# Performance work log

Measured on AMD Instinct MI355X. Metric: run time of the kernel, lower is better.

Reference implementation:

```python
import jax, jax.numpy as jnp
import numpy as np

S, N, E = 12, 16384, 262144        # timesteps, nodes, edges per timestep
DIN = DOUT = H = 128               # gcn in/out dim == lstm hidden (required by module)
B = 64                             # batch_size; N % B == 0


def setup_inputs() -> dict:
    key = jax.random.key(0)
    ks = jax.random.split(key, 10)
    return {
        "adj_indices": jax.random.randint(ks[0], (S, 2, E), 0, N, dtype=jnp.int32),
        "adj_values": jax.random.uniform(ks[1], (S, E), dtype=jnp.float32),
        "xs": jax.random.normal(ks[2], (S, N, DIN), dtype=jnp.float32),
        "gcn_weight": jax.random.normal(ks[3], (DIN, DOUT), dtype=jnp.float32) * 0.05,
        "gcn_bias": jnp.zeros((DOUT,), jnp.float32),
        "w_ih": jax.random.normal(ks[4], (4 * H, DOUT), dtype=jnp.float32) * 0.05,
        "w_hh": jax.random.normal(ks[5], (4 * H, H), dtype=jnp.float32) * 0.05,
        "b_ih": jnp.zeros((4 * H,), jnp.float32),
        "b_hh": jnp.zeros((4 * H,), jnp.float32),
        "h0": jax.random.normal(ks[6], (B, H), dtype=jnp.float32),
        "c0": jax.random.normal(ks[7], (B, H), dtype=jnp.float32),
    }


def reference(adj_indices, adj_values, xs, gcn_weight, gcn_bias,
              w_ih, w_hh, b_ih, b_hh, h0, c0):
    # --- GCN per timestep: relu(sparse_A @ (X @ W) + b) ---
    def gcn(idx, vals, x):
        support = x @ gcn_weight                      # [N, DOUT]
        msg = vals[:, None] * support[idx[1]]         # gather cols -> [E, DOUT]
        out = jax.ops.segment_sum(msg, idx[0], num_segments=N)  # scatter rows
        return jax.nn.relu(out + gcn_bias)

    cur = jax.vmap(gcn)(adj_indices, adj_values, xs)  # [S, N, DOUT]
    seq = cur.reshape(-1, B, DOUT)                    # [T=S*N/B, B, H]

    # --- single-layer LSTM (torch gate order: i, f, g, o) ---
    def step(carry, x_t):
        h, c = carry
        gates = x_t @ w_ih.T + b_ih + h @ w_hh.T + b_hh   # [B, 4H]
        i, f, g, o = jnp.split(gates, 4, axis=-1)
        c = jax.nn.sigmoid(f) * c + jax.nn.sigmoid(i) * jnp.tanh(g)
        h = jax.nn.sigmoid(o) * jnp.tanh(c)
        return (h, c), h

    _, hs = jax.lax.scan(step, (h0, c0), seq)         # [T, B, H]
    return hs
```

## Files before the change

kernel.cpp:

```cpp
#include <hip/hip_runtime.h>
#include <cstdint>
#include <cstddef>

#define SS 12
#define NN 16384
#define EE 262144
#define TT 3072

typedef _Float16 h2_t __attribute__((ext_vector_type(2)));
typedef short bf16x8 __attribute__((ext_vector_type(8)));
typedef float floatx4 __attribute__((ext_vector_type(4)));
typedef unsigned short ushortx8 __attribute__((ext_vector_type(8)));

__device__ __forceinline__ float fast_sig(float x) {
    float e = __builtin_amdgcn_exp2f(-1.442695041f * x);
    return __builtin_amdgcn_rcpf(1.f + e);
}
__device__ __forceinline__ float fast_tanh(float x) {
    float e = __builtin_amdgcn_exp2f(2.885390082f * x);
    return 1.f - 2.f * __builtin_amdgcn_rcpf(e + 1.f);
}
__device__ __forceinline__ unsigned short f2bf(float f) {
    unsigned int x = __float_as_uint(f);
    unsigned int r = (x + 0x7FFFu + ((x >> 16) & 1u)) >> 16;
    return (unsigned short)r;
}
__device__ __forceinline__ float bf2f(unsigned short u) {
    return __uint_as_float(((unsigned int)u) << 16);
}
__device__ __forceinline__ h2_t u2h(unsigned int u) {
    union { unsigned int u; h2_t h; } c; c.u = u; return c.h;
}

__global__ void k_zero(int* __restrict__ p) {
    p[blockIdx.x * 256 + threadIdx.x] = 0;
}

__global__ void k_count(const int* __restrict__ adj, int* __restrict__ counts) {
    int i = blockIdx.x * 256 + threadIdx.x;
    int t = i / EE, e = i - t * EE;
    int dst = adj[(size_t)t * 2 * EE + e];
    atomicAdd(&counts[t * NN + dst], 1);
}

__global__ void k_scan(const int* __restrict__ counts, int* __restrict__ offs,
                       int* __restrict__ cursor) {
    __shared__ int sums[1024];
    int t = blockIdx.x, tid = threadIdx.x;
    const int per = NN / 1024;
    int base = t * NN + tid * per;
    int local[16];
    int s = 0;
#pragma unroll
    for (int i = 0; i < per; i++) { local[i] = counts[base + i]; s += local[i]; }
    sums[tid] = s;
    __syncthreads();
    for (int off = 1; off < 1024; off <<= 1) {
        int v = (tid >= off) ? sums[tid - off] : 0;
        __syncthreads();
        sums[tid] += v;
        __syncthreads();
    }
    int run = sums[tid] - s;
#pragma unroll
    for (int i = 0; i < per; i++) { offs[base + i] = run; cursor[base + i] = run; run += local[i]; }
}

__global__ void k_scatter(const int* __restrict__ adj, const float* __restrict__ vals,
                          int* __restrict__ cursor, int2* __restrict__ edges) {
    int i = blockIdx.x * 256 + threadIdx.x;
    int t = i / EE, e = i - t * EE;
    int dst = adj[(size_t)t * 2 * EE + e];
    int src = adj[(size_t)t * 2 * EE + EE + e];
    float v = vals[(size_t)t * EE + e];
    int p = atomicAdd(&cursor[t * NN + dst], 1);
    edges[(size_t)t * EE + p] = make_int2(src, __float_as_int(v));
}

__global__ __launch_bounds__(256) void k_support(const float* __restrict__ xs,
                                                 const float* __restrict__ W,
                                                 unsigned short* __restrict__ sup) {
    __shared__ float Ash[64][128];
    __shared__ float Wsh[128][128];
    int tid = threadIdx.x;
    size_t rowbase = (size_t)blockIdx.x * 64;
    const float4* xa = (const float4*)(xs + rowbase * 128);
    float4* As = (float4*)&Ash[0][0];
#pragma unroll
    for (int q = 0; q < 8; q++) As[tid + q * 256] = xa[tid + q * 256];
    const float4* wg = (const float4*)W;
    float4* Ws = (float4*)&Wsh[0][0];
#pragma unroll
    for (int q = 0; q < 16; q++) Ws[tid + q * 256] = wg[tid + q * 256];
    __syncthreads();
    int jg = tid & 31, rg = tid >> 5;
    float acc[8][4];
#pragma unroll
    for (int i = 0; i < 8; i++)
#pragma unroll
        for (int j = 0; j < 4; j++) acc[i][j] = 0.f;
    for (int k4 = 0; k4 < 128; k4 += 4) {
        float4 a[8];
#pragma unroll
        for (int i = 0; i < 8; i++) a[i] = *(const float4*)&Ash[rg * 8 + i][k4];
#pragma unroll
        for (int kk = 0; kk < 4; kk++) {
            float4 wv = *(const float4*)&Wsh[k4 + kk][jg * 4];
#pragma unroll
            for (int i = 0; i < 8; i++) {
                float av = (kk == 0) ? a[i].x : (kk == 1) ? a[i].y : (kk == 2) ? a[i].z : a[i].w;
                acc[i][0] += av * wv.x; acc[i][1] += av * wv.y;
                acc[i][2] += av * wv.z; acc[i][3] += av * wv.w;
            }
        }
    }
#pragma unroll
    for (int i = 0; i < 8; i++) {
        ushort4 o;
        o.x = f2bf(acc[i][0]); o.y = f2bf(acc[i][1]);
        o.z = f2bf(acc[i][2]); o.w = f2bf(acc[i][3]);
        *(ushort4*)&sup[(rowbase + rg * 8 + i) * 128 + jg * 4] = o;
    }
}

__global__ __launch_bounds__(256) void k_gather(const int2* __restrict__ edges,
                         const int* __restrict__ offs,
                         const int* __restrict__ ends,
                         const unsigned short* __restrict__ sup,
                         const float* __restrict__ bias,
                         unsigned short* __restrict__ cur) {
    int bn = blockIdx.x * 4 + (threadIdx.x >> 6);
    bn = __builtin_amdgcn_readfirstlane(bn);
    int t = bn >> 14;
    int l = threadIdx.x & 63;
    int beg = offs[bn];
    int end = ends[bn];
    const unsigned short* supt = sup + (size_t)t * NN * 128;
    const int2* eg = edges + (size_t)t * EE;
    float acc0 = 0.f, acc1 = 0.f;
    int p = beg;
    for (; p + 3 < end; p += 4) {
        int2 e0 = eg[p], e1 = eg[p + 1], e2 = eg[p + 2], e3 = eg[p + 3];
        unsigned int u0 = *(const unsigned int*)&supt[(size_t)e0.x * 128 + 2 * l];
        unsigned int u1 = *(const unsigned int*)&supt[(size_t)e1.x * 128 + 2 * l];
        unsigned int u2 = *(const unsigned int*)&supt[(size_t)e2.x * 128 + 2 * l];
        unsigned int u3 = *(const unsigned int*)&supt[(size_t)e3.x * 128 + 2 * l];
        float w0 = __int_as_float(e0.y), w1 = __int_as_float(e1.y);
        float w2 = __int_as_float(e2.y), w3 = __int_as_float(e3.y);
        acc0 += w0 * bf2f((unsigned short)u0); acc1 += w0 * bf2f((unsigned short)(u0 >> 16));
        acc0 += w1 * bf2f((unsigned short)u1); acc1 += w1 * bf2f((unsigned short)(u1 >> 16));
        acc0 += w2 * bf2f((unsigned short)u2); acc1 += w2 * bf2f((unsigned short)(u2 >> 16));
        acc0 += w3 * bf2f((unsigned short)u3); acc1 += w3 * bf2f((unsigned short)(u3 >> 16));
    }
    for (; p < end; p++) {
        int2 e0 = eg[p];
        unsigned int u0 = *(const unsigned int*)&supt[(size_t)e0.x * 128 + 2 * l];
        float w0 = __int_as_float(e0.y);
        acc0 += w0 * bf2f((unsigned short)u0);
        acc1 += w0 * bf2f((unsigned short)(u0 >> 16));
    }
    float r0 = acc0 + bias[2 * l];
    float r1 = acc1 + bias[2 * l + 1];
    ushort2 o;
    o.x = f2bf(r0 > 0.f ? r0 : 0.f);
    o.y = f2bf(r1 > 0.f ? r1 : 0.f);
    *(ushort2*)&cur[(size_t)bn * 128 + 2 * l] = o;
}

__global__ __launch_bounds__(256) void k_xgates(const unsigned short* __restrict__ cur,
                                                const float* __restrict__ wih,
                                                const float* __restrict__ bih,
                                                const float* __restrict__ bhh,
                                                unsigned short* __restrict__ gx) {
    __shared__ __align__(16) unsigned short At[64][136];
    __shared__ __align__(16) unsigned short Bt[64][136];
    int tid = threadIdx.x;
    size_t rowbase = (size_t)blockIdx.x * 64;
    int gbase = blockIdx.y * 64;
#pragma unroll
    for (int q = 0; q < 4; q++) {
        int idx = tid + q * 256;
        int r = idx >> 4;
        int cc = (idx & 15) * 8;
        *(ushortx8*)&At[r][cc] = *(const ushortx8*)&cur[(rowbase + r) * 128 + cc];
    }
#pragma unroll
    for (int q = 0; q < 8; q++) {
        int idx = tid + q * 256;
        int r = idx >> 5;
        int c4 = (idx & 31) * 4;
        float4 v = *(const float4*)&wih[(size_t)(gbase + r) * 128 + c4];
        ushort4 o;
        o.x = f2bf(v.x); o.y = f2bf(v.y); o.z = f2bf(v.z); o.w = f2bf(v.w);
        *(ushort4*)&Bt[r][c4] = o;
    }
    __syncthreads();
    int wave = tid >> 6, lane = tid & 63;
    int m0 = wave * 16;
    int rin = lane & 15;
    int koff = (lane >> 4) * 8;
    floatx4 acc[4];
#pragma unroll
    for (int n = 0; n < 4; n++) acc[n] = (floatx4){0.f, 0.f, 0.f, 0.f};
#pragma unroll
    for (int kc = 0; kc < 4; kc++) {
        bf16x8 a = *(const bf16x8*)&At[m0 + rin][kc * 32 + koff];
#pragma unroll
        for (int n = 0; n < 4; n++) {
            bf16x8 b = *(const bf16x8*)&Bt[n * 16 + rin][kc * 32 + koff];
            acc[n] = __builtin_amdgcn_mfma_f32_16x16x32_bf16(a, b, acc[n], 0, 0, 0);
        }
    }
    int rq = (lane >> 4) * 4;
#pragma unroll
    for (int n = 0; n < 4; n++) {
        int gcol = gbase + n * 16 + rin;
        float bs = bih[gcol] + bhh[gcol];
#pragma unroll
        for (int i = 0; i < 4; i++) {
            size_t row = rowbase + m0 + rq + i;
            gx[row * 512 + gcol] = f2bf(acc[n][i] + bs);
        }
    }
}

__global__ __launch_bounds__(256, 1) void k_lstm(const unsigned short* __restrict__ gx,
                                                 const float* __restrict__ whh,
                                                 const float* __restrict__ h0,
                                                 const float* __restrict__ c0,
                                                 float* __restrict__ out) {
    __shared__ __align__(8) _Float16 hsh[128];
    __shared__ float gsh[512];
    int b = blockIdx.x, tid = threadIdx.x;
    int g1 = tid + 256;

    h2_t w0[64], w1[64];
    {
        const float4* r0 = (const float4*)(whh + (size_t)tid * 128);
        const float4* r1 = (const float4*)(whh + (size_t)g1 * 128);
#pragma unroll
        for (int q = 0; q < 32; q++) {
            float4 v = r0[q];
            h2_t p0; p0.x = (_Float16)v.x; p0.y = (_Float16)v.y;
            h2_t p1; p1.x = (_Float16)v.z; p1.y = (_Float16)v.w;
            w0[2 * q] = p0; w0[2 * q + 1] = p1;
        }
#pragma unroll
        for (int q = 0; q < 32; q++) {
            float4 v = r1[q];
            h2_t p0; p0.x = (_Float16)v.x; p0.y = (_Float16)v.y;
            h2_t p1; p1.x = (_Float16)v.z; p1.y = (_Float16)v.w;
            w1[2 * q] = p0; w1[2 * q + 1] = p1;
        }
    }
    float c = 0.f;
    if (tid < 128) {
        hsh[tid] = (_Float16)h0[(size_t)b * 128 + tid];
        c = c0[(size_t)b * 128 + tid];
    }
    __syncthreads();

    unsigned short nA0 = gx[(size_t)b * 512 + tid];
    unsigned short nA1 = gx[(size_t)b * 512 + g1];
    unsigned short nB0 = gx[((size_t)64 + b) * 512 + tid];
    unsigned short nB1 = gx[((size_t)64 + b) * 512 + g1];

    int lane = tid & 63;
    float hh[8];
    for (int t8 = 0; t8 < TT; t8 += 8) {
#pragma unroll
        for (int q = 0; q < 8; q++) {
            int t = t8 + q;
            float px0 = bf2f(nA0), px1 = bf2f(nA1);
            int tp2 = (t + 2 < TT) ? t + 2 : TT - 1;
            const unsigned short* gp = gx + ((size_t)tp2 * 64 + b) * 512;
            unsigned short nC0 = gp[tid];
            unsigned short nC1 = gp[g1];
            unsigned int hv = *(const unsigned int*)&hsh[lane * 2];
            float a00 = 0.f, a01 = 0.f, a10 = 0.f, a11 = 0.f;
#pragma unroll
            for (int mm = 0; mm < 64; mm += 2) {
                unsigned int s0 = __builtin_amdgcn_readlane(hv, mm);
                unsigned int s1 = __builtin_amdgcn_readlane(hv, mm + 1);
                a00 = __builtin_amdgcn_fdot2(w0[mm], u2h(s0), a00, false);
                a10 = __builtin_amdgcn_fdot2(w1[mm], u2h(s0), a10, false);
                a01 = __builtin_amdgcn_fdot2(w0[mm + 1], u2h(s1), a01, false);
                a11 = __builtin_amdgcn_fdot2(w1[mm + 1], u2h(s1), a11, false);
            }
            float r0 = a00 + a01 + px0;
            float r1 = a10 + a11 + px1;
            float act0 = fast_sig(r0);
            float act1 = (tid < 128) ? fast_tanh(r1) : fast_sig(r1);
            gsh[tid] = act0;
            gsh[g1] = act1;
            __syncthreads();
            if (tid < 128) {
                float ai = gsh[tid];
                float af = gsh[tid + 128];
                float ag = gsh[tid + 256];
                float ao = gsh[tid + 384];
                c = af * c + ai * ag;
                float hn = ao * fast_tanh(c);
                hh[q] = hn;
                hsh[tid] = (_Float16)hn;
            }
            __syncthreads();
            nA0 = nB0; nA1 = nB1; nB0 = nC0; nB1 = nC1;
        }
        if (tid < 128) {
#pragma unroll
            for (int q = 0; q < 8; q++)
                out[((size_t)(t8 + q) * 64 + b) * 128 + tid] = hh[q];
        }
    }
}

extern "C" void kernel_launch(void* const* d_in, const int* in_sizes, int n_in,
                              void* d_out, int out_size, void* d_ws, size_t ws_size,
                              hipStream_t stream) {
    const int* adj    = (const int*)d_in[0];
    const float* vals = (const float*)d_in[1];
    const float* xs   = (const float*)d_in[2];
    const float* gw   = (const float*)d_in[3];
    const float* gb   = (const float*)d_in[4];
    const float* wih  = (const float*)d_in[5];
    const float* whh  = (const float*)d_in[6];
    const float* bih  = (const float*)d_in[7];
    const float* bhh  = (const float*)d_in[8];
    const float* h0   = (const float*)d_in[9];
    const float* c0   = (const float*)d_in[10];
    float* out = (float*)d_out;

    char* ws = (char*)d_ws;
    unsigned short* cur = (unsigned short*)(ws);
    unsigned short* gx  = (unsigned short*)(ws + 50331648);
    unsigned short* sup = (unsigned short*)(ws + 50331648);
    int* counts         = (int*)(ws + 100663296);
    int* offs           = (int*)(ws + 101449728);
    int* cursor         = (int*)(ws + 102236160);
    int2* edges         = (int2*)(ws + 103022592);

    k_zero<<<(SS * NN) / 256, 256, 0, stream>>>(counts);
    k_count<<<(SS * EE) / 256, 256, 0, stream>>>(adj, counts);
    k_scan<<<SS, 1024, 0, stream>>>(counts, offs, cursor);
    k_scatter<<<(SS * EE) / 256, 256, 0, stream>>>(adj, vals, cursor, edges);
    k_support<<<(SS * NN) / 64, 256, 0, stream>>>(xs, gw, sup);
    k_gather<<<(SS * NN) / 4, 256, 0, stream>>>(edges, offs, cursor, sup, gb, cur);
    k_xgates<<<dim3((SS * NN) / 64, 8), 256, 0, stream>>>(cur, wih, bih, bhh, gx);
    k_lstm<<<64, 256, 0, stream>>>(gx, whh, h0, c0, out);
}
```

Before: 2.804 ms.

## Pair LSTM gates across adjacent lanes with DPP to drop a barrier per step

Gate rows are redistributed so each even/odd lane pair holds all four gates (i,f,g,o) of one hidden unit. The pair exchanges activations with a DPP quad-permute instead of going through shared memory, and the gx buffer is rewritten in a matching permuted column layout. Double-buffering the h vector in shared memory lets each timestep use one __syncthreads instead of two. Output is written directly each step rather than batched, and every lane now carries a cell state, with tanh computed as a scaled sigmoid.

Measured after the change: 2.564 ms. -8.6%, faster.

```diff
diff --git a/kernel.cpp b/kernel.cpp
--- a/kernel.cpp
+++ b/kernel.cpp
@@ -30,6 +30,10 @@
 }
 __device__ __forceinline__ h2_t u2h(unsigned int u) {
     union { unsigned int u; h2_t h; } c; c.u = u; return c.h;
+}
+__device__ __forceinline__ float dpp_xor1(float x) {
+    int i = __builtin_amdgcn_mov_dpp(__float_as_int(x), 0xB1, 0xF, 0xF, true);
+    return __int_as_float(i);
 }
 
 __global__ void k_zero(int* __restrict__ p) {
@@ -216,10 +220,12 @@
     for (int n = 0; n < 4; n++) {
         int gcol = gbase + n * 16 + rin;
         float bs = bih[gcol] + bhh[gcol];
+        int qg = gcol >> 7, jj = gcol & 127;
+        int slot = ((qg >> 1) << 8) | ((jj >> 5) << 6) | ((jj & 31) << 1) | (qg & 1);
 #pragma unroll
         for (int i = 0; i < 4; i++) {
             size_t row = rowbase + m0 + rq + i;
-            gx[row * 512 + gcol] = f2bf(acc[n][i] + bs);
+            gx[row * 512 + slot] = f2bf(acc[n][i] + bs);
         }
     }
 }
@@ -229,90 +235,88 @@
                                                  const float* __restrict__ h0,
                                                  const float* __restrict__ c0,
                                                  float* __restrict__ out) {
-    __shared__ __align__(8) _Float16 hsh[128];
-    __shared__ float gsh[512];
+    __shared__ __align__(8) _Float16 hsh[2][128];
     int b = blockIdx.x, tid = threadIdx.x;
-    int g1 = tid + 256;
+    int l = tid & 63, w = tid >> 6;
+    int j = w * 32 + (l >> 1);
+    bool even = (l & 1) == 0;
+    int gate0 = even ? j : 128 + j;
+    int gate1 = even ? 256 + j : 384 + j;
+    float Ss = even ? 2.f : 1.f;
+    float Aa = even ? 2.f : 1.f;
+    float Bb = even ? -1.f : 0.f;
 
     h2_t w0[64], w1[64];
     {
-        const float4* r0 = (const float4*)(whh + (size_t)tid * 128);
-        const float4* r1 = (const float4*)(whh + (size_t)g1 * 128);
+        const float4* r0p = (const float4*)(whh + (size_t)gate0 * 128);
+        const float4* r1p = (const float4*)(whh + (size_t)gate1 * 128);
 #pragma unroll
         for (int q = 0; q < 32; q++) {
-            float4 v = r0[q];
+            float4 v = r0p[q];
             h2_t p0; p0.x = (_Float16)v.x; p0.y = (_Float16)v.y;
             h2_t p1; p1.x = (_Float16)v.z; p1.y = (_Float16)v.w;
             w0[2 * q] = p0; w0[2 * q + 1] = p1;
         }
 #pragma unroll
         for (int q = 0; q < 32; q++) {
-            float4 v = r1[q];
+            float4 v = r1p[q];
             h2_t p0; p0.x = (_Float16)v.x; p0.y = (_Float16)v.y;
             h2_t p1; p1.x = (_Float16)v.z; p1.y = (_Float16)v.w;
             w1[2 * q] = p0; w1[2 * q + 1] = p1;
         }
     }
-    float c = 0.f;
-    if (tid < 128) {
-        hsh[tid] = (_Float16)h0[(size_t)b * 128 + tid];
-        c = c0[(size_t)b * 128 + tid];
-    }
+    float c = c0[(size_t)b * 128 + j];
+    if (tid < 128) hsh[0][tid] = (_Float16)h0[(size_t)b * 128 + tid];
     __syncthreads();
 
     unsigned short nA0 = gx[(size_t)b * 512 + tid];
-    unsigned short nA1 = gx[(size_t)b * 512 + g1];
+    unsigned short nA1 = gx[(size_t)b * 512 + 256 + tid];
     unsigned short nB0 = gx[((size_t)64 + b) * 512 + tid];
-    unsigned short nB1 = gx[((size_t)64 + b) * 512 + g1];
-
-    int lane = tid & 63;
-    float hh[8];
-    for (int t8 = 0; t8 < TT; t8 += 8) {
-#pragma unroll
-        for (int q = 0; q < 8; q++) {
-            int t = t8 + q;
-            float px0 = bf2f(nA0), px1 = bf2f(nA1);
-            int tp2 = (t + 2 < TT) ? t + 2 : TT - 1;
-            const unsigned short* gp = gx + ((size_t)tp2 * 64 + b) * 512;
-            unsigned short nC0 = gp[tid];
-            unsigned short nC1 = gp[g1];
-            unsigned int hv = *(const unsigned int*)&hsh[lane * 2];
-            float a00 = 0.f, a01 = 0.f, a10 = 0.f, a11 = 0.f;
-#pragma unroll
-            for (int mm = 0; mm < 64; mm += 2) {
-                unsigned int s0 = __builtin_amdgcn_readlane(hv, mm);
-                unsigned int s1 = __builtin_amdgcn_readlane(hv, mm + 1);
-                a00 = __builtin_amdgcn_fdot2(w0[mm], u2h(s0), a00, false);
-                a10 = __builtin_amdgcn_fdot2(w1[mm], u2h(s0), a10, false);
-                a01 = __builtin_amdgcn_fdot2(w0[mm + 1], u2h(s1), a01, false);
-                a11 = __builtin_amdgcn_fdot2(w1[mm + 1], u2h(s1), a11, false);
-            }
-            float r0 = a00 + a01 + px0;
-            float r1 = a10 + a11 + px1;
-            float act0 = fast_sig(r0);
-            float act1 = (tid < 128) ? fast_tanh(r1) : fast_sig(r1);
-            gsh[tid] = act0;
-            gsh[g1] = act1;
-            __syncthreads();
-            if (tid < 128) {
-                float ai = gsh[tid];
-                float af = gsh[tid + 128];
-                float ag = gsh[tid + 256];
-                float ao = gsh[tid + 384];
-                c = af * c + ai * ag;
-                float hn = ao * fast_tanh(c);
-                hh[q] = hn;
-                hsh[tid] = (_Float16)hn;
-            }
-            __syncthreads();
-            nA0 = nB0; nA1 = nB1; nB0 = nC0; nB1 = nC1;
-        }
-        if (tid < 128) {
-#pragma unroll
-            for (int q = 0; q < 8; q++)
-                out[((size_t)(t8 + q) * 64 + b) * 128 + tid] = hh[q];
-        }
-    }
+    unsigned short nB1 = gx[((size_t)64 + b) * 512 + 256 + tid];
+
+#define LSTM_STEP(T, RD, WR)                                               \
+    {                                                                      \
+        unsigned int hv = *(const unsigned int*)&hsh[RD][2 * l];           \
+        float px0 = bf2f(nA0), px1 = bf2f(nA1);                            \
+        int tp2 = ((T) + 2 < TT) ? (T) + 2 : TT - 1;                       \
+        const unsigned short* gp = gx + ((size_t)tp2 * 64 + b) * 512;      \
+        unsigned short nC0 = gp[tid];                                      \
+        unsigned short nC1 = gp[tid + 256];                                \
+        float a00 = 0.f, a01 = 0.f, a10 = 0.f, a11 = 0.f;                  \
+        _Pragma("unroll")                                                  \
+        for (int mm = 0; mm < 64; mm += 2) {                               \
+            unsigned int s0 = __builtin_amdgcn_readlane(hv, mm);           \
+            unsigned int s1 = __builtin_amdgcn_readlane(hv, mm + 1);       \
+            a00 = __builtin_amdgcn_fdot2(w0[mm], u2h(s0), a00, false);     \
+            a10 = __builtin_amdgcn_fdot2(w1[mm], u2h(s0), a10, false);     \
+            a01 = __builtin_amdgcn_fdot2(w0[mm + 1], u2h(s1), a01, false); \
+            a11 = __builtin_amdgcn_fdot2(w1[mm + 1], u2h(s1), a11, false); \
+        }                                                                  \
+        float r0 = a00 + a01 + px0;                                        \
+        float r1 = a10 + a11 + px1;                                        \
+        float act0 = fast_sig(r0);                                         \
+        float act1 = Aa * fast_sig(Ss * r1) + Bb;                          \
+        float q0 = dpp_xor1(act0);                                         \
+        float q1 = dpp_xor1(act1);                                         \
+        float gi = even ? act0 : q0;                                       \
+        float gf = even ? q0 : act0;                                       \
+        float gg = even ? act1 : q1;                                       \
+        float go = even ? q1 : act1;                                       \
+        c = gf * c + gi * gg;                                              \
+        float hn = go * fast_tanh(c);                                      \
+        if (even) {                                                        \
+            hsh[WR][j] = (_Float16)hn;                                     \
+            out[((size_t)(T) * 64 + b) * 128 + j] = hn;                    \
+        }                                                                  \
+        __syncthreads();                                                   \
+        nA0 = nB0; nA1 = nB1; nB0 = nC0; nB1 = nC1;                        \
+    }
+
+    for (int t = 0; t < TT; t += 2) {
+        LSTM_STEP(t, 0, 1);
+        LSTM_STEP(t + 1, 1, 0);
+    }
+#undef LSTM_STEP
 }
 
 extern "C" void kernel_launch(void* const* d_in, const int* in_sizes, int n_in,
```
